# Kernel tuning notes

Hardware: AMD Instinct MI355X
Metric: run time of the kernel (lower is better)

## Reference

```python
import jax, jax.numpy as jnp
import numpy as np

B = 4            # batch size (coords[:,0].max()+1 in the original)
C = 64           # NUM_BEV_FEATURES
NX, NY, NZ = 432, 496, 1
P_PER = 16000    # pillars per sample per bin
N_BINS = 3       # intersweep_sequence_length


def _make_coords(seed):
    # unique BEV cells per sample: strided modular arange (stride coprime with NX*NY)
    stride = 9973
    cells = (np.arange(P_PER, dtype=np.int64)[None, :] * stride + 17 * seed + 31 * np.arange(B)[:, None]) % (NX * NY)
    y = (cells // NX).reshape(-1)
    x = (cells % NX).reshape(-1)
    b = np.repeat(np.arange(B, dtype=np.int64), P_PER)
    z = np.zeros_like(b)
    return jnp.asarray(np.stack([b, z, y, x], axis=1), dtype=jnp.int32)  # [B*P_PER, 4]


def setup_inputs() -> dict:
    key = jax.random.key(0)
    inp = {}
    for i in range(N_BINS):
        key, kf = jax.random.split(key)
        inp[f"pillar_features_bin_{i}"] = jax.random.normal(kf, (B * P_PER, C), dtype=jnp.float32)
        inp[f"voxel_coords_bin_{i}"] = _make_coords(i)
    return inp


def _scatter_bin(pillars, coords):
    # coords layout: [batch, z, y, x]; per-sample flat index = z + y*nx + x (nz==1)
    c = coords.astype(jnp.int32)
    flat = c[:, 0] * (NY * NX) + c[:, 1] + c[:, 2] * NX + c[:, 3]  # batch-offset flattened index
    canvas = jnp.zeros((B * NY * NX, C), dtype=pillars.dtype).at[flat].set(pillars)
    return canvas.reshape(B, NY, NX, C).transpose(0, 3, 1, 2)  # [B, C, NY, NX]


def reference(pillar_features_bin_0, voxel_coords_bin_0,
              pillar_features_bin_1, voxel_coords_bin_1,
              pillar_features_bin_2, voxel_coords_bin_2):
    out0 = _scatter_bin(pillar_features_bin_0, voxel_coords_bin_0)
    out1 = _scatter_bin(pillar_features_bin_1, voxel_coords_bin_1)
    out2 = _scatter_bin(pillar_features_bin_2, voxel_coords_bin_2)
    return (out0, out1, out2)
```

## Files before the change

kernel.cpp:

```cpp
#include <hip/hip_runtime.h>

#define NX_ 432
#define NY_ 496
#define C_  64
#define B_  4
#define CELLS_ (NX_ * NY_)
#define PLANE_ ((size_t)CELLS_)
#define BATCH_STRIDE_ ((size_t)C_ * CELLS_)
#define BIN_STRIDE_   ((size_t)B_ * C_ * CELLS_)
#define MAP_BIN_ ((size_t)B_ * CELLS_)

typedef float vfloat4 __attribute__((ext_vector_type(4)));
typedef int   vint4   __attribute__((ext_vector_type(4)));

__global__ __launch_bounds__(256) void scatter_idx_kernel(
    const int* __restrict__ coords0,
    const int* __restrict__ coords1,
    const int* __restrict__ coords2,
    int* __restrict__ map, int npil)
{
    const int bin = blockIdx.y;
    const int p = blockIdx.x * 256 + threadIdx.x;
    if (p >= npil) return;
    const int* coords = (bin == 0) ? coords0 : (bin == 1) ? coords1 : coords2;
    vint4 c = ((const vint4*)coords)[p];
    size_t idx = (size_t)bin * MAP_BIN_ + (size_t)c.x * CELLS_ + c.y + c.z * NX_ + c.w;
    map[idx] = p;
}

__global__ __launch_bounds__(256) void gather_kernel(
    const float* __restrict__ pf0,
    const float* __restrict__ pf1,
    const float* __restrict__ pf2,
    const int* __restrict__ map,
    float* __restrict__ out)
{
    const int bin = blockIdx.z;
    const int b   = blockIdx.y;
    const int cell = blockIdx.x * 1024 + threadIdx.x * 4;
    if (cell >= CELLS_) return;

    const float* __restrict__ pf = (bin == 0) ? pf0 : (bin == 1) ? pf1 : pf2;

    const int* m = map + (size_t)bin * MAP_BIN_ + (size_t)b * CELLS_ + cell;
    vint4 idx = *(const vint4*)m;

    const bool v0 = idx.x >= 0, v1 = idx.y >= 0, v2 = idx.z >= 0, v3 = idx.w >= 0;
    const float* r0 = pf + (size_t)(v0 ? idx.x : 0) * C_;
    const float* r1 = pf + (size_t)(v1 ? idx.y : 0) * C_;
    const float* r2 = pf + (size_t)(v2 ? idx.z : 0) * C_;
    const float* r3 = pf + (size_t)(v3 ? idx.w : 0) * C_;

    float* o = out + (size_t)bin * BIN_STRIDE_ + (size_t)b * BATCH_STRIDE_ + cell;

#pragma unroll 4
    for (int c = 0; c < C_; ++c) {
        float x0 = r0[c];
        float x1 = r1[c];
        float x2 = r2[c];
        float x3 = r3[c];
        vfloat4 v;
        v.x = v0 ? x0 : 0.0f;
        v.y = v1 ? x1 : 0.0f;
        v.z = v2 ? x2 : 0.0f;
        v.w = v3 ? x3 : 0.0f;
        *(vfloat4*)(o + (size_t)c * PLANE_) = v;
    }
}

extern "C" void kernel_launch(void* const* d_in, const int* in_sizes, int n_in,
                              void* d_out, int out_size, void* d_ws, size_t ws_size,
                              hipStream_t stream) {
    const float* pf0 = (const float*)d_in[0];
    const int*   co0 = (const int*)d_in[1];
    const float* pf1 = (const float*)d_in[2];
    const int*   co1 = (const int*)d_in[3];
    const float* pf2 = (const float*)d_in[4];
    const int*   co2 = (const int*)d_in[5];
    float* out = (float*)d_out;

    const int npil = in_sizes[1] / 4;

    int* map = (int*)d_ws;
    const size_t map_bytes = 3 * MAP_BIN_ * sizeof(int);

    (void)hipMemsetAsync(map, 0xFF, map_bytes, stream);

    dim3 g1((npil + 255) / 256, 3, 1);
    scatter_idx_kernel<<<g1, 256, 0, stream>>>(co0, co1, co2, map, npil);

    dim3 g2((CELLS_ + 1023) / 1024, B_, 3);
    gather_kernel<<<g2, 256, 0, stream>>>(pf0, pf1, pf2, map, out);
}
```

Measured before the change: 701.1 us.

## Restructure gather so each block writes one channel plane with a prefetched index loop

The gather kernel now assigns one block per (channel, batch, bin) output plane. Each block loops over all cells in strides of 1024 and prefetches the next vector of map indices, instead of one block per 1024-cell chunk looping over all 64 channels. Output writes stay contiguous within a plane. The costs are that the map is re-read once per channel (64x more map traffic, mostly from cache), each pillar feature is read with a 256-byte stride, and the grid shrinks to 768 long-running blocks.

```diff
diff --git a/kernel.cpp b/kernel.cpp
--- a/kernel.cpp
+++ b/kernel.cpp
@@ -28,43 +28,49 @@
     map[idx] = p;
 }
 
-__global__ __launch_bounds__(256) void gather_kernel(
+__global__ __launch_bounds__(256) void gather_plane_kernel(
     const float* __restrict__ pf0,
     const float* __restrict__ pf1,
     const float* __restrict__ pf2,
     const int* __restrict__ map,
     float* __restrict__ out)
 {
+    const int c   = blockIdx.x;
+    const int b   = blockIdx.y;
     const int bin = blockIdx.z;
-    const int b   = blockIdx.y;
-    const int cell = blockIdx.x * 1024 + threadIdx.x * 4;
-    if (cell >= CELLS_) return;
 
-    const float* __restrict__ pf = (bin == 0) ? pf0 : (bin == 1) ? pf1 : pf2;
+    const float* __restrict__ pfb = (bin == 0) ? pf0 : (bin == 1) ? pf1 : pf2;
+    const float* __restrict__ pfc = pfb + c;
 
-    const int* m = map + (size_t)bin * MAP_BIN_ + (size_t)b * CELLS_ + cell;
-    vint4 idx = *(const vint4*)m;
+    const int* __restrict__ m = map + (size_t)bin * MAP_BIN_ + (size_t)b * CELLS_;
+    float* __restrict__ o = out + (size_t)bin * BIN_STRIDE_
+                                + (size_t)b * BATCH_STRIDE_
+                                + (size_t)c * PLANE_;
 
-    const bool v0 = idx.x >= 0, v1 = idx.y >= 0, v2 = idx.z >= 0, v3 = idx.w >= 0;
-    const float* r0 = pf + (size_t)(v0 ? idx.x : 0) * C_;
-    const float* r1 = pf + (size_t)(v1 ? idx.y : 0) * C_;
-    const float* r2 = pf + (size_t)(v2 ? idx.z : 0) * C_;
-    const float* r3 = pf + (size_t)(v3 ? idx.w : 0) * C_;
+    int cell = threadIdx.x * 4;
+    vint4 idx = *(const vint4*)(m + cell);
 
-    float* o = out + (size_t)bin * BIN_STRIDE_ + (size_t)b * BATCH_STRIDE_ + cell;
+    while (cell < CELLS_) {
+        const int next = cell + 1024;
+        vint4 nidx;
+        if (next < CELLS_)
+            nidx = *(const vint4*)(m + next);
 
-#pragma unroll 4
-    for (int c = 0; c < C_; ++c) {
-        float x0 = r0[c];
-        float x1 = r1[c];
-        float x2 = r2[c];
-        float x3 = r3[c];
-        vfloat4 v;
-        v.x = v0 ? x0 : 0.0f;
-        v.y = v1 ? x1 : 0.0f;
-        v.z = v2 ? x2 : 0.0f;
-        v.w = v3 ? x3 : 0.0f;
-        *(vfloat4*)(o + (size_t)c * PLANE_) = v;
+        const int i0 = idx.x, i1 = idx.y, i2 = idx.z, i3 = idx.w;
+        float x0 = pfc[(size_t)(i0 >= 0 ? i0 : 0) * C_];
+        float x1 = pfc[(size_t)(i1 >= 0 ? i1 : 0) * C_];
+        float x2 = pfc[(size_t)(i2 >= 0 ? i2 : 0) * C_];
+        float x3 = pfc[(size_t)(i3 >= 0 ? i3 : 0) * C_];
+
+        vfloat4 w;
+        w.x = i0 >= 0 ? x0 : 0.0f;
+        w.y = i1 >= 0 ? x1 : 0.0f;
+        w.z = i2 >= 0 ? x2 : 0.0f;
+        w.w = i3 >= 0 ? x3 : 0.0f;
+        *(vfloat4*)(o + cell) = w;
+
+        cell = next;
+        idx = nidx;
     }
 }
 
@@ -89,6 +95,6 @@
     dim3 g1((npil + 255) / 256, 3, 1);
     scatter_idx_kernel<<<g1, 256, 0, stream>>>(co0, co1, co2, map, npil);
 
-    dim3 g2((CELLS_ + 1023) / 1024, B_, 3);
-    gather_kernel<<<g2, 256, 0, stream>>>(pf0, pf1, pf2, map, out);
+    dim3 g2(C_, B_, 3);
+    gather_plane_kernel<<<g2, 256, 0, stream>>>(pf0, pf1, pf2, map, out);
 }
```

Measured after the change: 930.3 us. +32.7%, slower.

## Stage gathered pillar rows through LDS and load features as float4

Applied to the files above, without the earlier changes.

The gather kernel now reads each pillar row in float4 chunks of four channels, stages a 4-channel by 1024-cell tile in shared memory, and has each wavefront write one channel plane. The old version issued one scalar load per channel per pillar, scattered across rows. This change aims to cut the number of global load instructions and make loads wider while keeping output stores coalesced. It adds two barriers per channel group and LDS traffic, and the kernel is still dominated by writing the mostly-zero output.

```diff
diff --git a/kernel.cpp b/kernel.cpp
--- a/kernel.cpp
+++ b/kernel.cpp
@@ -28,21 +28,25 @@
     map[idx] = p;
 }
 
-__global__ __launch_bounds__(256) void gather_kernel(
+__global__ __launch_bounds__(256) void gather_lds_kernel(
     const float* __restrict__ pf0,
     const float* __restrict__ pf1,
     const float* __restrict__ pf2,
     const int* __restrict__ map,
     float* __restrict__ out)
 {
+    __shared__ float lds[4 * 1024];
+
     const int bin = blockIdx.z;
     const int b   = blockIdx.y;
-    const int cell = blockIdx.x * 1024 + threadIdx.x * 4;
-    if (cell >= CELLS_) return;
+    const int t   = threadIdx.x;
+    const int base = blockIdx.x * 1024;
 
     const float* __restrict__ pf = (bin == 0) ? pf0 : (bin == 1) ? pf1 : pf2;
 
-    const int* m = map + (size_t)bin * MAP_BIN_ + (size_t)b * CELLS_ + cell;
+    const int cell  = base + t * 4;
+    const int mcell = (cell < CELLS_) ? cell : 0;
+    const int* m = map + (size_t)bin * MAP_BIN_ + (size_t)b * CELLS_ + mcell;
     vint4 idx = *(const vint4*)m;
 
     const bool v0 = idx.x >= 0, v1 = idx.y >= 0, v2 = idx.z >= 0, v3 = idx.w >= 0;
@@ -51,20 +55,38 @@
     const float* r2 = pf + (size_t)(v2 ? idx.z : 0) * C_;
     const float* r3 = pf + (size_t)(v3 ? idx.w : 0) * C_;
 
-    float* o = out + (size_t)bin * BIN_STRIDE_ + (size_t)b * BATCH_STRIDE_ + cell;
+    const int wv = t >> 6;
+    const int ln = t & 63;
+    float* __restrict__ ob = out + (size_t)bin * BIN_STRIDE_
+                                 + (size_t)b * BATCH_STRIDE_;
 
-#pragma unroll 4
-    for (int c = 0; c < C_; ++c) {
-        float x0 = r0[c];
-        float x1 = r1[c];
-        float x2 = r2[c];
-        float x3 = r3[c];
-        vfloat4 v;
-        v.x = v0 ? x0 : 0.0f;
-        v.y = v1 ? x1 : 0.0f;
-        v.z = v2 ? x2 : 0.0f;
-        v.w = v3 ? x3 : 0.0f;
-        *(vfloat4*)(o + (size_t)c * PLANE_) = v;
+#pragma unroll
+    for (int g = 0; g < 16; ++g) {
+        vfloat4 x0 = *(const vfloat4*)(r0 + 4 * g);
+        vfloat4 x1 = *(const vfloat4*)(r1 + 4 * g);
+        vfloat4 x2 = *(const vfloat4*)(r2 + 4 * g);
+        vfloat4 x3 = *(const vfloat4*)(r3 + 4 * g);
+
+        __syncthreads();
+
+#pragma unroll
+        for (int cc = 0; cc < 4; ++cc) {
+            lds[cc * 1024 + t * 4 + 0] = v0 ? x0[cc] : 0.0f;
+            lds[cc * 1024 + t * 4 + 1] = v1 ? x1[cc] : 0.0f;
+            lds[cc * 1024 + t * 4 + 2] = v2 ? x2[cc] : 0.0f;
+            lds[cc * 1024 + t * 4 + 3] = v3 ? x3[cc] : 0.0f;
+        }
+
+        __syncthreads();
+
+        float* op = ob + (size_t)(4 * g + wv) * PLANE_;
+#pragma unroll
+        for (int k = 0; k < 4; ++k) {
+            const int oc = ln * 4 + 256 * k;
+            vfloat4 w = *(const vfloat4*)&lds[wv * 1024 + oc];
+            if (base + oc < CELLS_)
+                *(vfloat4*)(op + base + oc) = w;
+        }
     }
 }
 
@@ -90,5 +112,5 @@
     scatter_idx_kernel<<<g1, 256, 0, stream>>>(co0, co1, co2, map, npil);
 
     dim3 g2((CELLS_ + 1023) / 1024, B_, 3);
-    gather_kernel<<<g2, 256, 0, stream>>>(pf0, pf1, pf2, map, out);
+    gather_lds_kernel<<<g2, 256, 0, stream>>>(pf0, pf1, pf2, map, out);
 }
```

Measured after the change: 700.9 us. No clear change (-0.0%).

## Split gather kernel across channel groups with vectorized feature loads

Applied to the files above, without the earlier changes.

The gather kernel now assigns each block a group of four channels instead of all 64, and the grid gains a channel-group dimension (16 groups), with bin and batch folded into z. Each thread loads one float4 per source pillar rather than 64 scalar loads, then writes four output planes. This raises parallelism and memory-level concurrency for a write-bandwidth-bound kernel. In exchange, the index map is re-read 16 times, and the pillar rows are fetched by 16 different blocks.

```diff
diff --git a/kernel.cpp b/kernel.cpp
--- a/kernel.cpp
+++ b/kernel.cpp
@@ -28,15 +28,18 @@
     map[idx] = p;
 }
 
-__global__ __launch_bounds__(256) void gather_kernel(
+__global__ __launch_bounds__(256) void gather_split_kernel(
     const float* __restrict__ pf0,
     const float* __restrict__ pf1,
     const float* __restrict__ pf2,
     const int* __restrict__ map,
     float* __restrict__ out)
 {
-    const int bin = blockIdx.z;
-    const int b   = blockIdx.y;
+    const int g   = blockIdx.y;
+    const int zb  = blockIdx.z;
+    const int bin = zb >> 2;
+    const int b   = zb & 3;
+
     const int cell = blockIdx.x * 1024 + threadIdx.x * 4;
     if (cell >= CELLS_) return;
 
@@ -46,25 +49,21 @@
     vint4 idx = *(const vint4*)m;
 
     const bool v0 = idx.x >= 0, v1 = idx.y >= 0, v2 = idx.z >= 0, v3 = idx.w >= 0;
-    const float* r0 = pf + (size_t)(v0 ? idx.x : 0) * C_;
-    const float* r1 = pf + (size_t)(v1 ? idx.y : 0) * C_;
-    const float* r2 = pf + (size_t)(v2 ? idx.z : 0) * C_;
-    const float* r3 = pf + (size_t)(v3 ? idx.w : 0) * C_;
+    const vfloat4 x0 = *(const vfloat4*)(pf + (size_t)(v0 ? idx.x : 0) * C_ + 4 * g);
+    const vfloat4 x1 = *(const vfloat4*)(pf + (size_t)(v1 ? idx.y : 0) * C_ + 4 * g);
+    const vfloat4 x2 = *(const vfloat4*)(pf + (size_t)(v2 ? idx.z : 0) * C_ + 4 * g);
+    const vfloat4 x3 = *(const vfloat4*)(pf + (size_t)(v3 ? idx.w : 0) * C_ + 4 * g);
 
     float* o = out + (size_t)bin * BIN_STRIDE_ + (size_t)b * BATCH_STRIDE_ + cell;
 
-#pragma unroll 4
-    for (int c = 0; c < C_; ++c) {
-        float x0 = r0[c];
-        float x1 = r1[c];
-        float x2 = r2[c];
-        float x3 = r3[c];
-        vfloat4 v;
-        v.x = v0 ? x0 : 0.0f;
-        v.y = v1 ? x1 : 0.0f;
-        v.z = v2 ? x2 : 0.0f;
-        v.w = v3 ? x3 : 0.0f;
-        *(vfloat4*)(o + (size_t)c * PLANE_) = v;
+#pragma unroll
+    for (int q = 0; q < 4; ++q) {
+        vfloat4 w;
+        w.x = v0 ? x0[q] : 0.0f;
+        w.y = v1 ? x1[q] : 0.0f;
+        w.z = v2 ? x2[q] : 0.0f;
+        w.w = v3 ? x3[q] : 0.0f;
+        *(vfloat4*)(o + (size_t)(4 * g + q) * PLANE_) = w;
     }
 }
 
@@ -89,6 +88,6 @@
     dim3 g1((npil + 255) / 256, 3, 1);
     scatter_idx_kernel<<<g1, 256, 0, stream>>>(co0, co1, co2, map, npil);
 
-    dim3 g2((CELLS_ + 1023) / 1024, B_, 3);
-    gather_kernel<<<g2, 256, 0, stream>>>(pf0, pf1, pf2, map, out);
+    dim3 g2((CELLS_ + 1023) / 1024, C_ / 4, 3 * B_);
+    gather_split_kernel<<<g2, 256, 0, stream>>>(pf0, pf1, pf2, map, out);
 }
```

Result: faster. 684.8 us (median of 2 runs) (-2.3%).
